# Kernel optimization log

Hardware: AMD Instinct MI355X
Metric: run time of the kernel (lower is better)

## Reference

```python
import jax, jax.numpy as jnp
import numpy as np

CHUNK = 64
EMA_DECAY = 0.99


def setup_inputs() -> dict:
    key = jax.random.key(0)
    ks = jax.random.split(key, 4)
    Bsz, S, H, P, N = 2, 4096, 16, 64, 128
    X = jax.random.normal(ks[0], (Bsz, S, H, P), jnp.float32)
    # negative log-decay rates, as in Mamba-2 (A = -softplus(...) style)
    A = -jnp.abs(jax.random.normal(ks[1], (Bsz, S, H), jnp.float32)) * 0.1
    Bm = jax.random.normal(ks[2], (Bsz, S, H, N), jnp.float32) / np.sqrt(N)
    Cm = jax.random.normal(ks[3], (Bsz, S, H, N), jnp.float32) / np.sqrt(N)
    # ChunkedSurpriseGate parameters / buffers
    log2_alpha_base = jnp.full((H,), -0.15, jnp.float32)
    log2_beta = jnp.zeros((H,), jnp.float32)
    surprise_ema = jnp.ones((H,), jnp.float32)
    return {"X": X, "A": A, "Bm": Bm, "Cm": Cm,
            "log2_alpha_base": log2_alpha_base, "log2_beta": log2_beta,
            "surprise_ema": surprise_ema}


def _chunked_surprise_ssd(X, A, Bm, Cm, log2_alpha_base, log2_beta, surprise_ema):
    Bsz, S, H, P = X.shape
    N = Bm.shape[-1]
    cs = CHUNK
    nC = S // cs  # seqlen chosen divisible by chunk_size (no padding branch)

    # [B, nC, cs, H, ...] -> chunk-major [nC, B, H, cs, ...] for lax.scan
    Xc = X.reshape(Bsz, nC, cs, H, P).transpose(1, 0, 3, 2, 4)   # [nC,B,H,cs,P]
    Ac = A.reshape(Bsz, nC, cs, H).transpose(1, 0, 3, 2)          # [nC,B,H,cs]
    Bc = Bm.reshape(Bsz, nC, cs, H, N).transpose(1, 0, 3, 2, 4)   # [nC,B,H,cs,N]
    Cc = Cm.reshape(Bsz, nC, cs, H, N).transpose(1, 0, 3, 2, 4)   # [nC,B,H,cs,N]

    idx = jnp.arange(cs)
    tri = idx[:, None] >= idx[None, :]  # causal mask for decay matrix L

    # gate constants (per-head)
    alpha_base = 1.0 - jnp.exp2(jnp.clip(log2_alpha_base, -3.32, -0.015))  # [H]
    beta = jnp.exp2(jnp.clip(log2_beta, -2.0, 2.0))                         # [H]

    def step(carry, xs):
        h_prev, h_before, decay_prev, ema = carry
        c, X_c, A_c, B_c, C_c = xs
        first = c == 0

        # --- delayed state-based surprise: ||h_prev - decay_prev * h_before||^2
        err = jnp.mean((h_prev - decay_prev[..., None, None] * h_before) ** 2,
                       axis=(-2, -1))  # [B,H]
        # EMA update (training=True path; torch does it under no_grad)
        ema_new = jax.lax.stop_gradient(EMA_DECAY * ema + (1.0 - EMA_DECAY) * jnp.mean(err, axis=0))
        normalized = err / (ema_new[None, :] + 1e-6)                # [B,H]
        boost = jax.nn.relu(jnp.tanh(beta[None, :] * normalized))
        alpha = jnp.clip(alpha_base[None, :] + (1.0 - alpha_base[None, :]) * boost,
                         0.01, 0.999)
        # torch: decay_scale = (1-alpha).mean().item()  -> detached scalar
        ds = jax.lax.stop_gradient(jnp.mean(1.0 - alpha))
        decay_scale = jnp.where(first, jnp.float32(1.0), ds)
        ema_out = jnp.where(first, ema, ema_new)  # no gate call on chunk 0

        # --- single-chunk SSD ---
        Acs = jnp.cumsum(A_c * decay_scale, axis=-1)                 # [B,H,cs]
        # causal decay matrix L[i,j] = exp(Acs[i]-Acs[j]) for i>=j
        L = jnp.where(tri, jnp.exp(Acs[..., :, None] - Acs[..., None, :]), 0.0)
        CB = jnp.einsum('bhin,bhjn->bhij', C_c, B_c)
        Y_intra = jnp.einsum('bhij,bhjd->bhid', L * CB, X_c)
        decay_from_start = jnp.exp(Acs)                               # [B,H,cs]
        Y_inter = jnp.einsum('bhin,bhnd,bhi->bhid', C_c, h_prev, decay_from_start)
        decay_to_end = jnp.exp(Acs[..., -1:] - Acs)                   # [B,H,cs]
        h_contrib = jnp.einsum('bhtn,bhtd,bht->bhnd', B_c, X_c, decay_to_end)
        decay_total = jnp.exp(Acs[..., -1])                           # [B,H]
        h_end = decay_total[..., None, None] * h_prev + h_contrib

        return (h_end, h_prev, decay_total, ema_out), Y_intra + Y_inter

    h0 = jnp.zeros((Bsz, H, N, P), X.dtype)
    carry0 = (h0, h0, jnp.ones((Bsz, H), X.dtype), surprise_ema)
    xs = (jnp.arange(nC), Xc, Ac, Bc, Cc)
    _, Ys = jax.lax.scan(step, carry0, xs)  # [nC,B,H,cs,P]

    # stack dim=2, permute(0,2,3,1,4), reshape -> [B,S,H,P]
    Y = Ys.transpose(1, 0, 3, 2, 4).reshape(Bsz, S, H, P)
    return Y


def reference(X, A, Bm, Cm, log2_alpha_base, log2_beta, surprise_ema):
    return _chunked_surprise_ssd(X, A, Bm, Cm, log2_alpha_base, log2_beta, surprise_ema)
```

## Files before the change

### kernel.cpp

```cpp
#include <hip/hip_runtime.h>
#include <math.h>


#define CSZ 64
#define NCH 64
#define NHD 16
#define PD  64
#define ND  128
#define BHN 32
#define NTILES 2048
#define GGRID 64
#define SEQ 4096

#define WS_S   0
#define WS_EG  131072
#define WS_DS  262144
#define WS_HC  262400

using bf16x8 = __attribute__((ext_vector_type(8))) short;
using f32x4  = __attribute__((ext_vector_type(4))) float;

__device__ __forceinline__ short f2bf(float f) {
  union { float f; unsigned u; } v; v.f = f;
  unsigned r = (v.u + 0x7FFFu + ((v.u >> 16) & 1u)) >> 16;
  return (short)r;
}

__device__ __forceinline__ float bf2f(short s) {
  union { float f; unsigned u; } v;
  v.u = ((unsigned)(unsigned short)s) << 16;
  return v.f;
}

__device__ __forceinline__ void split4(float4 v, short4& hi, short4& lo) {
  hi.x = f2bf(v.x); lo.x = f2bf(v.x - bf2f(hi.x));
  hi.y = f2bf(v.y); lo.y = f2bf(v.y - bf2f(hi.y));
  hi.z = f2bf(v.z); lo.z = f2bf(v.z - bf2f(hi.z));
  hi.w = f2bf(v.w); lo.w = f2bf(v.w - bf2f(hi.w));
}

__global__ __launch_bounds__(256) void k_gramerr(
    const float* __restrict__ X, const float* __restrict__ A,
    const float* __restrict__ Bm, float* __restrict__ ws)
{
  __shared__ __align__(16) short BhiS[64*136];
  __shared__ __align__(16) short BloS[64*136];
  __shared__ __align__(16) short XhiS[64*72];
  __shared__ __align__(16) short XloS[64*72];
  __shared__ float Sl[CSZ];
  __shared__ float Zl[CSZ];
  short* Mhi = BhiS;
  short* Mlo = BloS;
  short* Uhi = XhiS;
  short* Ulo = XloS;

  const int tile = blockIdx.x;
  const int c  = tile & 63;
  const int bh = tile >> 6;
  const int b = bh >> 4, h = bh & 15;
  const int tid = threadIdx.x;

  if (tid < CSZ) {
    float v = A[(size_t)(b*SEQ + c*CSZ + tid)*NHD + h];
    #pragma unroll
    for (int d = 1; d < 64; d <<= 1) {
      float n = __shfl_up(v, d);
      if (tid >= d) v += n;
    }
    Sl[tid] = v;
    ws[WS_S + tile*CSZ + tid] = v;
  }

  {
    const float* Bbase = Bm + ((size_t)(b*SEQ + c*CSZ)*NHD + h)*ND;
    #pragma unroll
    for (int qq = 0; qq < 8; ++qq) {
      int lin = qq*256 + tid;
      int t = lin >> 5, n4 = (lin & 31)*4;
      float4 v = *(const float4*)(Bbase + (size_t)t*(NHD*ND) + n4);
      short4 hi, lo; split4(v, hi, lo);
      *(short4*)&BhiS[t*136 + n4] = hi;
      *(short4*)&BloS[t*136 + n4] = lo;
    }
    const float* Xbase = X + ((size_t)(b*SEQ + c*CSZ)*NHD + h)*PD;
    #pragma unroll
    for (int qq = 0; qq < 4; ++qq) {
      int lin = qq*256 + tid;
      int t = lin >> 4, p4 = (lin & 15)*4;
      float4 v = *(const float4*)(Xbase + (size_t)t*(NHD*PD) + p4);
      short4 hi, lo; split4(v, hi, lo);
      *(short4*)&XhiS[t*72 + p4] = hi;
      *(short4*)&XloS[t*72 + p4] = lo;
    }
  }
  __syncthreads();

  if (tid < CSZ) Zl[tid] = Sl[63] - Sl[tid];

  const int w = tid >> 6;
  const int lane = tid & 63;
  const int m = lane & 15, q = lane >> 4;

  f32x4 z4 = {0.f,0.f,0.f,0.f};
  f32x4 gb[4], gx[4];
  #pragma unroll
  for (int i = 0; i < 4; ++i) { gb[i] = z4; gx[i] = z4; }

  #pragma unroll
  for (int kk = 0; kk < 4; ++kk) {
    const int ao = (w*16+m)*136 + kk*32 + q*8;
    bf16x8 ah = *(bf16x8*)&BhiS[ao];
    bf16x8 al = *(bf16x8*)&BloS[ao];
    #pragma unroll
    for (int ct = 0; ct < 4; ++ct) {
      const int bo = (ct*16+m)*136 + kk*32 + q*8;
      bf16x8 bhv = *(bf16x8*)&BhiS[bo];
      bf16x8 blv = *(bf16x8*)&BloS[bo];
      gb[ct] = __builtin_amdgcn_mfma_f32_16x16x32_bf16(ah, bhv, gb[ct], 0,0,0);
      gb[ct] = __builtin_amdgcn_mfma_f32_16x16x32_bf16(ah, blv, gb[ct], 0,0,0);
      gb[ct] = __builtin_amdgcn_mfma_f32_16x16x32_bf16(al, bhv, gb[ct], 0,0,0);
    }
  }
  #pragma unroll
  for (int kk = 0; kk < 2; ++kk) {
    const int ao = (w*16+m)*72 + kk*32 + q*8;
    bf16x8 ah = *(bf16x8*)&XhiS[ao];
    bf16x8 al = *(bf16x8*)&XloS[ao];
    #pragma unroll
    for (int ct = 0; ct < 4; ++ct) {
      const int bo = (ct*16+m)*72 + kk*32 + q*8;
      bf16x8 bhv = *(bf16x8*)&XhiS[bo];
      bf16x8 blv = *(bf16x8*)&XloS[bo];
      gx[ct] = __builtin_amdgcn_mfma_f32_16x16x32_bf16(ah, bhv, gx[ct], 0,0,0);
      gx[ct] = __builtin_amdgcn_mfma_f32_16x16x32_bf16(ah, blv, gx[ct], 0,0,0);
      gx[ct] = __builtin_amdgcn_mfma_f32_16x16x32_bf16(al, bhv, gx[ct], 0,0,0);
    }
  }
  __syncthreads();

  #pragma unroll
  for (int ct = 0; ct < 4; ++ct)
    #pragma unroll
    for (int r = 0; r < 4; ++r) {
      int i = w*16 + q*4 + r;
      int j = ct*16 + m;
      float mvf = gb[ct][r]*gx[ct][r]*(1.0f/8192.0f);
      short mh = f2bf(mvf);
      Mhi[i*72 + j] = mh;
      Mlo[i*72 + j] = f2bf(mvf - bf2f(mh));
    }
  #pragma unroll
  for (int qq = 0; qq < 16; ++qq) {
    int idx = qq*256 + tid;
    int g = idx >> 6, t = idx & 63;
    float u = expf(((float)g*(1.0f/63.0f))*Zl[t]);
    short uh = f2bf(u);
    Uhi[g*72 + t] = uh;
    Ulo[g*72 + t] = f2bf(u - bf2f(uh));
  }
  __syncthreads();

  f32x4 wv4[4];
  #pragma unroll
  for (int i = 0; i < 4; ++i) wv4[i] = z4;
  #pragma unroll
  for (int kk = 0; kk < 2; ++kk) {
    const int ao = (w*16+m)*72 + kk*32 + q*8;
    bf16x8 uh = *(bf16x8*)&Uhi[ao];
    bf16x8 ul = *(bf16x8*)&Ulo[ao];
    #pragma unroll
    for (int ct = 0; ct < 4; ++ct) {
      const int bo = (ct*16+m)*72 + kk*32 + q*8;
      bf16x8 mh = *(bf16x8*)&Mhi[bo];
      bf16x8 ml = *(bf16x8*)&Mlo[bo];
      wv4[ct] = __builtin_amdgcn_mfma_f32_16x16x32_bf16(uh, mh, wv4[ct], 0,0,0);
      wv4[ct] = __builtin_amdgcn_mfma_f32_16x16x32_bf16(uh, ml, wv4[ct], 0,0,0);
      wv4[ct] = __builtin_amdgcn_mfma_f32_16x16x32_bf16(ul, mh, wv4[ct], 0,0,0);
    }
  }

  #pragma unroll
  for (int r = 0; r < 4; ++r) {
    int g = w*16 + q*4 + r;
    float e = 0.f;
    #pragma unroll
    for (int ct = 0; ct < 4; ++ct) {
      int t = ct*16 + m;
      float uval = bf2f(Uhi[g*72 + t]) + bf2f(Ulo[g*72 + t]);
      e += wv4[ct][r] * uval;
    }
    e += __shfl_xor(e, 1);
    e += __shfl_xor(e, 2);
    e += __shfl_xor(e, 4);
    e += __shfl_xor(e, 8);
    if (m == 0) ws[WS_EG + (c*GGRID + g)*BHN + bh] = e;
  }
}

__global__ __launch_bounds__(64) void k_gate(
    const float* __restrict__ l2ab, const float* __restrict__ l2b,
    const float* __restrict__ sema, float* __restrict__ ws)
{
  __shared__ float EGs[2][GGRID*BHN];
  const int lane = threadIdx.x;
  const int h = lane & 15;
  float ab = 0.f, bt = 1.f, ema = 0.f;
  if (lane < NHD) {
    float la = fminf(fmaxf(l2ab[lane], -3.32f), -0.015f);
    ab = 1.0f - exp2f(la);
    float lb = fminf(fmaxf(l2b[lane], -2.0f), 2.0f);
    bt = exp2f(lb);
    ema = sema[lane];
  }
  const float ab_bh = __shfl(ab, h);
  const float bt_bh = __shfl(bt, h);
  const float* EG = ws + WS_EG;
  {
    const float4* src = (const float4*)EG;
    float4* dst = (float4*)EGs[0];
    #pragma unroll
    for (int r = 0; r < 8; ++r) dst[r*64 + lane] = src[r*64 + lane];
  }
  float ds_prev = 1.0f;
  if (lane == 0) ws[WS_DS + 0] = 1.0f;
  for (int c = 1; c < NCH; ++c) {
    const int cur = (c - 1) & 1;
    float4 pf[8];
    if (c < NCH-1) {
      const float4* src = (const float4*)(EG + (size_t)c*(GGRID*BHN));
      #pragma unroll
      for (int r = 0; r < 8; ++r) pf[r] = src[r*64 + lane];
    }
    float x = ds_prev * 63.0f;
    int ib = (int)floorf(x);
    ib = max(1, min(61, ib));
    float u = x - (float)ib;
    float err = 0.f;
    if (lane < BHN) {
      const float* p = &EGs[cur][(ib-1)*BHN + lane];
      float ym1 = p[0], y0 = p[32], y1 = p[64], y2 = p[96];
      err = ym1*(u*(u-1.f)*(u-2.f))*(-1.f/6.f)
          + y0 *((u+1.f)*(u-1.f)*(u-2.f))*(0.5f)
          + y1 *((u+1.f)*u*(u-2.f))*(-0.5f)
          + y2 *((u+1.f)*u*(u-1.f))*(1.f/6.f);
    }
    float e0 = __shfl(err, h);
    float e1 = __shfl(err, 16 + h);
    float ema_new = 0.99f*ema + 0.01f*0.5f*(e0 + e1);
    float emv = __shfl(ema_new, h);
    float oma = 0.f;
    if (lane < BHN) {
      float normalized = err / (emv + 1e-6f);
      float boost = fmaxf(tanhf(bt_bh*normalized), 0.f);
      float alpha = ab_bh + (1.f - ab_bh)*boost;
      alpha = fminf(fmaxf(alpha, 0.01f), 0.999f);
      oma = 1.f - alpha;
    }
    float s = oma;
    s += __shfl_xor(s, 1);  s += __shfl_xor(s, 2);  s += __shfl_xor(s, 4);
    s += __shfl_xor(s, 8);  s += __shfl_xor(s, 16);
    float ds = __shfl(s, 0) * (1.0f/32.0f);
    if (lane < NHD) ema = ema_new;
    if (lane == 0) ws[WS_DS + c] = ds;
    ds_prev = ds;
    if (c < NCH-1) {
      float4* dst = (float4*)EGs[c & 1];
      #pragma unroll
      for (int r = 0; r < 8; ++r) dst[r*64 + lane] = pf[r];
    }
  }
}

__global__ __launch_bounds__(256, 3) void k_chunk(
    const float* __restrict__ X, const float* __restrict__ Bm,
    const float* __restrict__ Cm, float* __restrict__ ws,
    float* __restrict__ Y)
{
  __shared__ short Bs[64*136];
  __shared__ short BsTw[128*72];
  __shared__ short XsT[64*72];
  __shared__ float Acs[CSZ];
  __shared__ float Wl[CSZ];
  short* Es = Bs;

  const int tile = blockIdx.x;
  const int c  = tile & 63;
  const int bh = tile >> 6;
  const int b = bh >> 4, h = bh & 15;
  const int tid = threadIdx.x;
  const int w = tid >> 6;
  const int lane = tid & 63;
  const int m = lane & 15, q = lane >> 4;

  const float* Bbase = Bm + ((size_t)(b*SEQ + c*CSZ)*NHD + h)*ND;
  const float* Cbase = Cm + ((size_t)(b*SEQ + c*CSZ)*NHD + h)*ND;
  const float* Xbase = X  + ((size_t)(b*SEQ + c*CSZ)*NHD + h)*PD;

  const float* crow = Cbase + (size_t)(w*16 + m)*(NHD*ND);
  float4 cflo[4], cfhi[4];
  #pragma unroll
  for (int kk = 0; kk < 4; ++kk) {
    cflo[kk] = *(const float4*)(crow + kk*32 + q*8);
    cfhi[kk] = *(const float4*)(crow + kk*32 + q*8 + 4);
  }

  const float dsc = ws[WS_DS + c];
  if (tid < CSZ) {
    float sv  = ws[WS_S + tile*CSZ + tid];
    float s63 = ws[WS_S + tile*CSZ + 63];
    Acs[tid] = dsc*sv;
    Wl[tid]  = expf(dsc*(s63 - sv));
  }
  __syncthreads();

  #pragma unroll
  for (int qq = 0; qq < 8; ++qq) {
    int lin = qq*256 + tid;
    int t = lin >> 5, n4 = (lin & 31)*4;
    float4 bv = *(const float4*)(Bbase + (size_t)t*(NHD*ND) + n4);
    short4 bs4; bs4.x=f2bf(bv.x); bs4.y=f2bf(bv.y); bs4.z=f2bf(bv.z); bs4.w=f2bf(bv.w);
    *(short4*)&Bs[t*136 + n4] = bs4;
    float wt = Wl[t];
    BsTw[(n4+0)*72 + t] = f2bf(bv.x*wt);
    BsTw[(n4+1)*72 + t] = f2bf(bv.y*wt);
    BsTw[(n4+2)*72 + t] = f2bf(bv.z*wt);
    BsTw[(n4+3)*72 + t] = f2bf(bv.w*wt);
  }
  #pragma unroll
  for (int qq = 0; qq < 4; ++qq) {
    int lin = qq*256 + tid;
    int t = lin >> 4, p4 = (lin & 15)*4;
    float4 xv = *(const float4*)(Xbase + (size_t)t*(NHD*PD) + p4);
    XsT[(p4+0)*72 + t] = f2bf(xv.x);
    XsT[(p4+1)*72 + t] = f2bf(xv.y);
    XsT[(p4+2)*72 + t] = f2bf(xv.z);
    XsT[(p4+3)*72 + t] = f2bf(xv.w);
  }
  __syncthreads();

  bf16x8 af[4];
  #pragma unroll
  for (int kk = 0; kk < 4; ++kk) {
    bf16x8 t;
    t[0]=f2bf(cflo[kk].x); t[1]=f2bf(cflo[kk].y); t[2]=f2bf(cflo[kk].z); t[3]=f2bf(cflo[kk].w);
    t[4]=f2bf(cfhi[kk].x); t[5]=f2bf(cfhi[kk].y); t[6]=f2bf(cfhi[kk].z); t[7]=f2bf(cfhi[kk].w);
    af[kk] = t;
  }

  f32x4 acc0 = {0.f,0.f,0.f,0.f}, acc1 = acc0, acc2 = acc0, acc3 = acc0;
  #pragma unroll
  for (int kk = 0; kk < 4; ++kk) {
    bf16x8 b0 = *(bf16x8*)&Bs[( 0+m)*136 + kk*32 + q*8];
    bf16x8 b1 = *(bf16x8*)&Bs[(16+m)*136 + kk*32 + q*8];
    bf16x8 b2 = *(bf16x8*)&Bs[(32+m)*136 + kk*32 + q*8];
    bf16x8 b3 = *(bf16x8*)&Bs[(48+m)*136 + kk*32 + q*8];
    acc0 = __builtin_amdgcn_mfma_f32_16x16x32_bf16(af[kk], b0, acc0, 0,0,0);
    acc1 = __builtin_amdgcn_mfma_f32_16x16x32_bf16(af[kk], b1, acc1, 0,0,0);
    acc2 = __builtin_amdgcn_mfma_f32_16x16x32_bf16(af[kk], b2, acc2, 0,0,0);
    acc3 = __builtin_amdgcn_mfma_f32_16x16x32_bf16(af[kk], b3, acc3, 0,0,0);
  }
  __syncthreads();

  {
    f32x4 accs[4] = {acc0, acc1, acc2, acc3};
    #pragma unroll
    for (int ct = 0; ct < 4; ++ct) {
      int j = ct*16 + m;
      float aj = Acs[j];
      #pragma unroll
      for (int r = 0; r < 4; ++r) {
        int i = w*16 + q*4 + r;
        float v = (i >= j) ? expf(Acs[i]-aj)*accs[ct][r] : 0.f;
        Es[i*72 + j] = f2bf(v);
      }
    }
  }

  f32x4 h00={0.f,0.f,0.f,0.f}, h01=h00, h02=h00, h03=h00;
  f32x4 h10=h00, h11=h00, h12=h00, h13=h00;
  #pragma unroll
  for (int kk = 0; kk < 2; ++kk) {
    bf16x8 a0 = *(bf16x8*)&BsTw[((2*w+0)*16+m)*72 + kk*32 + q*8];
    bf16x8 a1 = *(bf16x8*)&BsTw[((2*w+1)*16+m)*72 + kk*32 + q*8];
    bf16x8 x0 = *(bf16x8*)&XsT[( 0+m)*72 + kk*32 + q*8];
    bf16x8 x1 = *(bf16x8*)&XsT[(16+m)*72 + kk*32 + q*8];
    bf16x8 x2 = *(bf16x8*)&XsT[(32+m)*72 + kk*32 + q*8];
    bf16x8 x3 = *(bf16x8*)&XsT[(48+m)*72 + kk*32 + q*8];
    h00 = __builtin_amdgcn_mfma_f32_16x16x32_bf16(a0, x0, h00, 0,0,0);
    h01 = __builtin_amdgcn_mfma_f32_16x16x32_bf16(a0, x1, h01, 0,0,0);
    h02 = __builtin_amdgcn_mfma_f32_16x16x32_bf16(a0, x2, h02, 0,0,0);
    h03 = __builtin_amdgcn_mfma_f32_16x16x32_bf16(a0, x3, h03, 0,0,0);
    h10 = __builtin_amdgcn_mfma_f32_16x16x32_bf16(a1, x0, h10, 0,0,0);
    h11 = __builtin_amdgcn_mfma_f32_16x16x32_bf16(a1, x1, h11, 0,0,0);
    h12 = __builtin_amdgcn_mfma_f32_16x16x32_bf16(a1, x2, h12, 0,0,0);
    h13 = __builtin_amdgcn_mfma_f32_16x16x32_bf16(a1, x3, h13, 0,0,0);
  }

  f32x4 y0={0.f,0.f,0.f,0.f}, y1=y0, y2=y0, y3=y0;
  #pragma unroll
  for (int kk = 0; kk < 2; ++kk) {
    bf16x8 ef = *(bf16x8*)&Es[(w*16+m)*72 + kk*32 + q*8];
    bf16x8 x0 = *(bf16x8*)&XsT[( 0+m)*72 + kk*32 + q*8];
    bf16x8 x1 = *(bf16x8*)&XsT[(16+m)*72 + kk*32 + q*8];
    bf16x8 x2 = *(bf16x8*)&XsT[(32+m)*72 + kk*32 + q*8];
    bf16x8 x3 = *(bf16x8*)&XsT[(48+m)*72 + kk*32 + q*8];
    y0 = __builtin_amdgcn_mfma_f32_16x16x32_bf16(ef, x0, y0, 0,0,0);
    y1 = __builtin_amdgcn_mfma_f32_16x16x32_bf16(ef, x1, y1, 0,0,0);
    y2 = __builtin_amdgcn_mfma_f32_16x16x32_bf16(ef, x2, y2, 0,0,0);
    y3 = __builtin_amdgcn_mfma_f32_16x16x32_bf16(ef, x3, y3, 0,0,0);
  }

  {
    float* Ybase = Y + ((size_t)(b*SEQ + c*CSZ)*NHD + h)*PD;
    f32x4 ys[4] = {y0, y1, y2, y3};
    #pragma unroll
    for (int r = 0; r < 4; ++r) {
      int i = w*16 + q*4 + r;
      #pragma unroll
      for (int ct = 0; ct < 4; ++ct)
        Ybase[(size_t)i*(NHD*PD) + ct*16 + m] = ys[ct][r];
    }
  }
  {
    float* hcp = ws + WS_HC + (size_t)tile*(ND*PD);
    f32x4 hs[2][4] = {{h00,h01,h02,h03},{h10,h11,h12,h13}};
    #pragma unroll
    for (int nt = 0; nt < 2; ++nt)
      #pragma unroll
      for (int r = 0; r < 4; ++r) {
        int n = (2*w+nt)*16 + q*4 + r;
        #pragma unroll
        for (int pt = 0; pt < 4; ++pt)
          hcp[n*PD + pt*16 + m] = hs[nt][pt][r];
      }
  }
}

__global__ __launch_bounds__(256) void k_scan(float* __restrict__ ws)
{
  __shared__ float dtbl[NCH];
  const int bh = blockIdx.x >> 5, part = blockIdx.x & 31;
  const int tid = threadIdx.x;
  if (tid < NCH) {
    float s63 = ws[WS_S + (bh*NCH + tid)*CSZ + 63];
    dtbl[tid] = expf(ws[WS_DS + tid]*s63);
  }
  __syncthreads();
  float* base = ws + WS_HC + (size_t)bh*(NCH*ND*PD) + part*256 + tid;
  float hacc = 0.f;
  #pragma unroll 1
  for (int c = 0; c < NCH; ++c) {
    float* p = base + (size_t)c*(ND*PD);
    float v = *p;
    *p = hacc;
    hacc = dtbl[c]*hacc + v;
  }
}

__global__ __launch_bounds__(256, 4) void k_inter(
    const float* __restrict__ Cm, float* __restrict__ ws,
    float* __restrict__ Y)
{
  __shared__ short Cs[64*136];
  __shared__ short HsT[64*136];
  __shared__ float Dfs[CSZ];

  const int tile = blockIdx.x;
  const int c  = tile & 63;
  const int bh = tile >> 6;
  const int b = bh >> 4, h = bh & 15;
  const int tid = threadIdx.x;

  const float dsc = ws[WS_DS + c];
  if (tid < CSZ) Dfs[tid] = expf(dsc*ws[WS_S + tile*CSZ + tid]);

  const float* Cbase = Cm + ((size_t)(b*SEQ + c*CSZ)*NHD + h)*ND;
  const float* hp = ws + WS_HC + (size_t)tile*(ND*PD);
  #pragma unroll
  for (int qq = 0; qq < 8; ++qq) {
    int lin = qq*256 + tid;
    int t = lin >> 5, n4 = (lin & 31)*4;
    float4 cv = *(const float4*)(Cbase + (size_t)t*(NHD*ND) + n4);
    short4 cs4; cs4.x=f2bf(cv.x); cs4.y=f2bf(cv.y); cs4.z=f2bf(cv.z); cs4.w=f2bf(cv.w);
    *(short4*)&Cs[t*136 + n4] = cs4;
    int n = lin >> 4, p4 = (lin & 15)*4;
    float4 hv = *(const float4*)(hp + (size_t)lin*4);
    HsT[(p4+0)*136 + n] = f2bf(hv.x);
    HsT[(p4+1)*136 + n] = f2bf(hv.y);
    HsT[(p4+2)*136 + n] = f2bf(hv.z);
    HsT[(p4+3)*136 + n] = f2bf(hv.w);
  }
  __syncthreads();

  const int w = tid >> 6;
  const int lane = tid & 63;
  const int m = lane & 15, q = lane >> 4;

  f32x4 a0 = {0.f,0.f,0.f,0.f}, a1 = a0, a2 = a0, a3 = a0;
  #pragma unroll
  for (int kk = 0; kk < 4; ++kk) {
    bf16x8 cf = *(bf16x8*)&Cs[(w*16+m)*136 + kk*32 + q*8];
    bf16x8 hb0 = *(bf16x8*)&HsT[( 0+m)*136 + kk*32 + q*8];
    bf16x8 hb1 = *(bf16x8*)&HsT[(16+m)*136 + kk*32 + q*8];
    bf16x8 hb2 = *(bf16x8*)&HsT[(32+m)*136 + kk*32 + q*8];
    bf16x8 hb3 = *(bf16x8*)&HsT[(48+m)*136 + kk*32 + q*8];
    a0 = __builtin_amdgcn_mfma_f32_16x16x32_bf16(cf, hb0, a0, 0,0,0);
    a1 = __builtin_amdgcn_mfma_f32_16x16x32_bf16(cf, hb1, a1, 0,0,0);
    a2 = __builtin_amdgcn_mfma_f32_16x16x32_bf16(cf, hb2, a2, 0,0,0);
    a3 = __builtin_amdgcn_mfma_f32_16x16x32_bf16(cf, hb3, a3, 0,0,0);
  }

  float* Ybase = Y + ((size_t)(b*SEQ + c*CSZ)*NHD + h)*PD;
  f32x4 as[4] = {a0, a1, a2, a3};
  #pragma unroll
  for (int r = 0; r < 4; ++r) {
    int i = w*16 + q*4 + r;
    float d = Dfs[i];
    #pragma unroll
    for (int ct = 0; ct < 4; ++ct) {
      size_t idx = (size_t)i*(NHD*PD) + ct*16 + m;
      Ybase[idx] += d*as[ct][r];
    }
  }
}

extern "C" void kernel_launch(void* const* d_in, const int* in_sizes, int n_in,
                              void* d_out, int out_size, void* d_ws, size_t ws_size,
                              hipStream_t stream) {
  const float* X    = (const float*)d_in[0];
  const float* A    = (const float*)d_in[1];
  const float* Bm   = (const float*)d_in[2];
  const float* Cm   = (const float*)d_in[3];
  const float* l2ab = (const float*)d_in[4];
  const float* l2b  = (const float*)d_in[5];
  const float* sema = (const float*)d_in[6];
  float* Y  = (float*)d_out;
  float* ws = (float*)d_ws;

  hipLaunchKernelGGL(k_gramerr, dim3(NTILES), dim3(256), 0, stream, X, A, Bm, ws);
  hipLaunchKernelGGL(k_gate,    dim3(1),      dim3(64),  0, stream, l2ab, l2b, sema, ws);
  hipLaunchKernelGGL(k_chunk,   dim3(NTILES), dim3(256), 0, stream, X, Bm, Cm, ws, Y);
  hipLaunchKernelGGL(k_scan,    dim3(1024),   dim3(256), 0, stream, ws);
  hipLaunchKernelGGL(k_inter,   dim3(NTILES), dim3(256), 0, stream, Cm, ws, Y);
}
```

Before: 367.4 us.

## Stream gate error slabs into an 8-deep LDS ring via direct global-to-LDS loads

The serial gate kernel previously double-buffered each per-chunk error slab through registers, then copied it into shared memory. It now issues asynchronous global_load_lds transfers straight into an 8-slot shared-memory ring, six slabs ahead, and waits with explicit vmcnt counters. This is meant to hide global memory latency on the single-wave sequential scan and to drop the register-to-LDS copy. The cost is a hand-tuned waitcnt scheme that must match the number of outstanding loads exactly, plus 64KB of LDS for the ring.

```diff
diff --git a/kernel.cpp b/kernel.cpp
--- a/kernel.cpp
+++ b/kernel.cpp
@@ -201,9 +201,11 @@
     const float* __restrict__ l2ab, const float* __restrict__ l2b,
     const float* __restrict__ sema, float* __restrict__ ws)
 {
-  __shared__ float EGs[2][GGRID*BHN];
+  __shared__ __align__(16) float ring[8*GGRID*BHN];
   const int lane = threadIdx.x;
   const int h = lane & 15;
+  const float* EG = ws + WS_EG;
+
   float ab = 0.f, bt = 1.f, ema = 0.f;
   if (lane < NHD) {
     float la = fminf(fmaxf(l2ab[lane], -3.32f), -0.015f);
@@ -214,30 +216,44 @@
   }
   const float ab_bh = __shfl(ab, h);
   const float bt_bh = __shfl(bt, h);
-  const float* EG = ws + WS_EG;
-  {
-    const float4* src = (const float4*)EG;
-    float4* dst = (float4*)EGs[0];
-    #pragma unroll
-    for (int r = 0; r < 8; ++r) dst[r*64 + lane] = src[r*64 + lane];
-  }
+
+  #define ISSUE_SLAB(s)                                                        \
+    {                                                                          \
+      const float* gsrc = EG + (size_t)(s)*(GGRID*BHN) + lane*4;               \
+      float* lbase = ring + ((s) & 7)*(GGRID*BHN);                             \
+      _Pragma("unroll")                                                        \
+      for (int r = 0; r < 8; ++r) {                                            \
+        __builtin_amdgcn_global_load_lds(                                      \
+            (const __attribute__((address_space(1))) void*)(gsrc + r*256),     \
+            (__attribute__((address_space(3))) void*)(lbase + r*256),          \
+            16, 0, 0);                                                         \
+      }                                                                        \
+    }
+
+  #pragma unroll
+  for (int s = 0; s < 6; ++s) ISSUE_SLAB(s);
+
   float ds_prev = 1.0f;
   if (lane == 0) ws[WS_DS + 0] = 1.0f;
+
   for (int c = 1; c < NCH; ++c) {
-    const int cur = (c - 1) & 1;
-    float4 pf[8];
-    if (c < NCH-1) {
-      const float4* src = (const float4*)(EG + (size_t)c*(GGRID*BHN));
-      #pragma unroll
-      for (int r = 0; r < 8; ++r) pf[r] = src[r*64 + lane];
-    }
+    const int j = c - 1;
+    if (j + 6 <= 62) ISSUE_SLAB(j + 6);
+    if (j <= 56) {
+      asm volatile("s_waitcnt vmcnt(48)" ::: "memory");
+    } else {
+      asm volatile("s_waitcnt vmcnt(0)" ::: "memory");
+    }
+    __builtin_amdgcn_sched_barrier(0);
+    const float* slab = ring + (j & 7)*(GGRID*BHN);
+
     float x = ds_prev * 63.0f;
     int ib = (int)floorf(x);
     ib = max(1, min(61, ib));
     float u = x - (float)ib;
     float err = 0.f;
     if (lane < BHN) {
-      const float* p = &EGs[cur][(ib-1)*BHN + lane];
+      const float* p = slab + (ib-1)*BHN + lane;
       float ym1 = p[0], y0 = p[32], y1 = p[64], y2 = p[96];
       err = ym1*(u*(u-1.f)*(u-2.f))*(-1.f/6.f)
           + y0 *((u+1.f)*(u-1.f)*(u-2.f))*(0.5f)
@@ -263,12 +279,8 @@
     if (lane < NHD) ema = ema_new;
     if (lane == 0) ws[WS_DS + c] = ds;
     ds_prev = ds;
-    if (c < NCH-1) {
-      float4* dst = (float4*)EGs[c & 1];
-      #pragma unroll
-      for (int r = 0; r < 8; ++r) dst[r*64 + lane] = pf[r];
-    }
-  }
+  }
+  #undef ISSUE_SLAB
 }
 
 __global__ __launch_bounds__(256, 3) void k_chunk(
```

Result: faster. 336.0 us (-8.6%).
